# Optimization experiments

Hardware: AMD Instinct MI355X
Metric: run time of the kernel (lower is better)

## Reference

```python
import jax, jax.numpy as jnp
import numpy as np

B, D, H, C = 8192, 384, 256, 6
K_MIN, K_MAX = 4, 16
LN_EPS = 1e-5


def setup_inputs() -> dict:
    key = jax.random.key(0)
    ks = jax.random.split(key, 6)
    s = lambda k, shape: (jax.random.normal(k, shape, jnp.float32) * 0.05)
    return {
        "x": jax.random.normal(ks[0], (B, D), jnp.float32),
        "W_proj": s(ks[1], (D, H)), "b_proj": jnp.zeros((H,), jnp.float32),
        "W_tau": s(ks[2], (D, 1)), "b_tau": jnp.zeros((1,), jnp.float32),
        "W_res": s(ks[3], (H, H)), "b_res": jnp.zeros((H,), jnp.float32),
        "ln_g": jnp.ones((H,), jnp.float32), "ln_b": jnp.zeros((H,), jnp.float32),
        "W_fc": s(ks[4], (H, C)), "b_fc": jnp.zeros((C,), jnp.float32),
    }


def reference(x, W_proj, b_proj, W_tau, b_tau, W_res, b_res, ln_g, ln_b, W_fc, b_fc):
    # adaptive k per sample (torch path casts to int -> non-differentiable)
    tau = jax.nn.sigmoid(x @ W_tau + b_tau)[:, 0]                      # [B]
    k = jax.lax.stop_gradient(
        jnp.clip(jnp.round(K_MAX - (K_MAX - K_MIN) * tau), 1, K_MAX)
    ).astype(jnp.int32)                                                # [B]

    # pairwise squared distances (same nearest-neighbor ordering as cdist)
    sq = jnp.sum(x * x, axis=-1)                                       # [B]
    d2 = sq[:, None] + sq[None, :] - 2.0 * (x @ x.T)                   # [B,B]
    _, idx = jax.lax.top_k(-jax.lax.stop_gradient(d2), K_MAX)          # [B,K_MAX] nearest (incl. self)

    h = jax.nn.relu(x @ W_proj + b_proj)                               # [B,H]

    # ragged top-k mean via fixed K_MAX gather + position mask
    gathered = h[idx]                                                  # [B,K_MAX,H]
    mask = (jnp.arange(K_MAX)[None, :] < k[:, None]).astype(h.dtype)   # [B,K_MAX]
    agg = jnp.einsum('bkh,bk->bh', gathered, mask) / k[:, None].astype(h.dtype)

    r = jax.nn.relu(agg @ W_res + b_res)                               # [B,H]
    z = h + r
    mu = jnp.mean(z, axis=-1, keepdims=True)
    var = jnp.var(z, axis=-1, keepdims=True)
    zn = (z - mu) / jnp.sqrt(var + LN_EPS)
    return (zn * ln_g + ln_b) @ W_fc + b_fc                            # [B,C]
```

## Files before the change

kernel.cpp:

```cpp
#include <hip/hip_runtime.h>
#include <hip/hip_fp16.h>
#include <math.h>

#define NROWS 8192
#define DDIM 384
#define HDIM 256
#define CDIM 6
#define LN_EPS 1e-5f
#define DSTR 138

typedef short bf16x8 __attribute__((ext_vector_type(8)));
typedef float f32x4 __attribute__((ext_vector_type(4)));
typedef unsigned short u16x8 __attribute__((ext_vector_type(8)));
typedef unsigned short u16x4 __attribute__((ext_vector_type(4)));
typedef unsigned short u16x2 __attribute__((ext_vector_type(2)));

__device__ __forceinline__ bool dj_better(float d1, int j1, float d2, int j2) {
    return (d1 < d2) || (d1 == d2 && j1 < j2);
}

__device__ __forceinline__ unsigned int umin_(unsigned int a, unsigned int b) { return a < b ? a : b; }
__device__ __forceinline__ unsigned int umax_(unsigned int a, unsigned int b) { return a > b ? a : b; }

__device__ __forceinline__ unsigned short map16f(float v) {
    union { _Float16 f; unsigned short u; } c;
    c.f = (_Float16)v;
    unsigned short b = c.u;
    return (unsigned short)(b ^ (unsigned short)((((short)b) >> 15) | 0x8000));
}

__device__ __forceinline__ unsigned short rne_bf16(float v) {
    unsigned int u = __float_as_uint(v);
    u += 0x7fffu + ((u >> 16) & 1u);
    return (unsigned short)(u >> 16);
}

__device__ __forceinline__ void ins8(
    unsigned int& s0, unsigned int& s1, unsigned int& s2, unsigned int& s3,
    unsigned int& s4, unsigned int& s5, unsigned int& s6, unsigned int& s7,
    unsigned int& m, unsigned int key)
{
    if (key < m) {
        s0 = (s0 == m) ? key : s0;
        s1 = (s1 == m) ? key : s1;
        s2 = (s2 == m) ? key : s2;
        s3 = (s3 == m) ? key : s3;
        s4 = (s4 == m) ? key : s4;
        s5 = (s5 == m) ? key : s5;
        s6 = (s6 == m) ? key : s6;
        s7 = (s7 == m) ? key : s7;
        m = umax_(umax_(umax_(s0, s1), umax_(s2, s3)),
                  umax_(umax_(s4, s5), umax_(s6, s7)));
    }
}

__device__ __forceinline__ unsigned int max8_(
    unsigned int s0, unsigned int s1, unsigned int s2, unsigned int s3,
    unsigned int s4, unsigned int s5, unsigned int s6, unsigned int s7)
{
    return umax_(umax_(umax_(s0, s1), umax_(s2, s3)),
                 umax_(umax_(s4, s5), umax_(s6, s7)));
}

__global__ void __launch_bounds__(256) prep_kernel(
    const float* __restrict__ x, const float* __restrict__ W_tau,
    const float* __restrict__ b_tau, unsigned short* __restrict__ xb,
    float* __restrict__ sq, int* __restrict__ kk,
    const float* __restrict__ Wp, unsigned short* __restrict__ wpT,
    const float* __restrict__ Wr, unsigned short* __restrict__ wrT)
{
    int tid = threadIdx.x;
    if (blockIdx.x < NROWS / 4) {
        int wave = tid >> 6, lane = tid & 63;
        int row = blockIdx.x * 4 + wave;
        const float* xr = x + (size_t)row * DDIM;
        unsigned short* xbr = xb + (size_t)row * DDIM;
        float s = 0.f, tp = 0.f;
        #pragma unroll
        for (int q = 0; q < 6; ++q) {
            float v = xr[lane + 64 * q];
            xbr[lane + 64 * q] = rne_bf16(v);
            s = fmaf(v, v, s);
            tp = fmaf(v, W_tau[lane + 64 * q], tp);
        }
        #pragma unroll
        for (int off = 32; off > 0; off >>= 1) {
            s += __shfl_xor(s, off);
            tp += __shfl_xor(tp, off);
        }
        if (lane == 0) {
            sq[row] = s;
            float u = tp + b_tau[0];
            float tau = 1.f / (1.f + expf(-u));
            float kf = rintf(16.f - 12.f * tau);
            int k = (int)kf;
            k = min(16, max(1, k));
            kk[row] = k;
        }
    } else {
        int i = (blockIdx.x - NROWS / 4) * 256 + tid;
        if (i < DDIM * HDIM) {
            int k = i / HDIM, n = i % HDIM;
            wpT[(size_t)n * DDIM + k] = rne_bf16(Wp[i]);
        } else {
            int j = i - DDIM * HDIM;
            if (j < HDIM * HDIM) {
                int k = j / HDIM, n = j % HDIM;
                wrT[(size_t)n * HDIM + k] = rne_bf16(Wr[j]);
            }
        }
    }
}

__global__ void __launch_bounds__(256) mfma_gemm_bias_relu_kernel(
    const unsigned short* __restrict__ A, const unsigned short* __restrict__ WT,
    const float* __restrict__ bias, float* __restrict__ out,
    unsigned short* __restrict__ hb, int K)
{
    __shared__ unsigned short Abuf[128 * 32];
    __shared__ unsigned short Bbuf[128 * 32];

    const int tid = threadIdx.x;
    const int wave = tid >> 6;
    const int rowbase = blockIdx.x * 128;
    const int nbase = blockIdx.y * 128;
    const int lane = tid & 63;
    const int wr = (wave >> 1) * 64;
    const int wc = (wave & 1) * 64;
    const int m16 = lane & 15;
    const int kq = lane >> 4;

    const int er0 = tid >> 2;
    const int er1 = 64 + (tid >> 2);
    const int eko = tid & 3;

    f32x4 acc[4][4];
    #pragma unroll
    for (int a = 0; a < 4; ++a)
        #pragma unroll
        for (int b = 0; b < 4; ++b)
            acc[a][b] = (f32x4){0.f, 0.f, 0.f, 0.f};

    for (int kb = 0; kb < K / 32; ++kb) {
        const int k0 = kb * 32;
        __syncthreads();
        __builtin_amdgcn_global_load_lds(
            (const __attribute__((address_space(1))) void*)(A + (size_t)(rowbase + er0) * K + k0 + eko * 8),
            (__attribute__((address_space(3))) void*)((char*)Abuf + (wave * 64) * 16), 16, 0, 0);
        __builtin_amdgcn_global_load_lds(
            (const __attribute__((address_space(1))) void*)(A + (size_t)(rowbase + er1) * K + k0 + eko * 8),
            (__attribute__((address_space(3))) void*)((char*)Abuf + (256 + wave * 64) * 16), 16, 0, 0);
        __builtin_amdgcn_global_load_lds(
            (const __attribute__((address_space(1))) void*)(WT + (size_t)(nbase + er0) * K + k0 + eko * 8),
            (__attribute__((address_space(3))) void*)((char*)Bbuf + (wave * 64) * 16), 16, 0, 0);
        __builtin_amdgcn_global_load_lds(
            (const __attribute__((address_space(1))) void*)(WT + (size_t)(nbase + er1) * K + k0 + eko * 8),
            (__attribute__((address_space(3))) void*)((char*)Bbuf + (256 + wave * 64) * 16), 16, 0, 0);
        __syncthreads();

        bf16x8 af[4], bfr[4];
        #pragma unroll
        for (int s = 0; s < 4; ++s) {
            af[s]  = *(const bf16x8*)&Abuf[(wr + s * 16 + m16) * 32 + kq * 8];
            bfr[s] = *(const bf16x8*)&Bbuf[(wc + s * 16 + m16) * 32 + kq * 8];
        }
        #pragma unroll
        for (int si = 0; si < 4; ++si)
            #pragma unroll
            for (int sj = 0; sj < 4; ++sj)
                acc[si][sj] = __builtin_amdgcn_mfma_f32_16x16x32_bf16(
                    af[si], bfr[sj], acc[si][sj], 0, 0, 0);
    }

    #pragma unroll
    for (int sj = 0; sj < 4; ++sj) {
        int c = nbase + wc + sj * 16 + m16;
        float bc = bias[c];
        #pragma unroll
        for (int si = 0; si < 4; ++si) {
            int r = rowbase + wr + si * 16 + kq * 4;
            #pragma unroll
            for (int v = 0; v < 4; ++v) {
                float val = fmaxf(acc[si][sj][v] + bc, 0.f);
                out[(size_t)(r + v) * HDIM + c] = val;
                if (hb) hb[(size_t)(r + v) * HDIM + c] = rne_bf16(val);
            }
        }
    }
}

__global__ void __launch_bounds__(256) dist_topk_kernel(
    const unsigned short* __restrict__ xb, const float* __restrict__ sq,
    unsigned int* __restrict__ keys)
{
    __shared__ unsigned short Abuf[128 * 32];
    __shared__ unsigned short Bbuf[128 * 32];
    __shared__ __align__(16) unsigned short Dt[128 * DSTR];

    int t = blockIdx.x;
    int bi = (int)((sqrtf(8.f * (float)t + 1.f) - 1.f) * 0.5f);
    while ((bi + 1) * (bi + 2) / 2 <= t) ++bi;
    while (bi * (bi + 1) / 2 > t) --bi;
    int bj = t - bi * (bi + 1) / 2;

    const int tid = threadIdx.x;
    const int wave = tid >> 6;
    const int lane = tid & 63;
    const int rowbase = bi * 128;
    const int colbase = bj * 128;
    const int wr = (wave >> 1) * 64;
    const int wc = (wave & 1) * 64;
    const int m16 = lane & 15;
    const int kq = lane >> 4;

    const int er0 = tid >> 2;
    const int er1 = 64 + (tid >> 2);
    const int eko = tid & 3;

    f32x4 acc[4][4];
    #pragma unroll
    for (int a = 0; a < 4; ++a)
        #pragma unroll
        for (int b = 0; b < 4; ++b)
            acc[a][b] = (f32x4){0.f, 0.f, 0.f, 0.f};

    for (int kb = 0; kb < DDIM / 32; ++kb) {
        const int k0 = kb * 32;
        __syncthreads();
        __builtin_amdgcn_global_load_lds(
            (const __attribute__((address_space(1))) void*)(xb + (size_t)(rowbase + er0) * DDIM + k0 + eko * 8),
            (__attribute__((address_space(3))) void*)((char*)Abuf + (wave * 64) * 16), 16, 0, 0);
        __builtin_amdgcn_global_load_lds(
            (const __attribute__((address_space(1))) void*)(xb + (size_t)(rowbase + er1) * DDIM + k0 + eko * 8),
            (__attribute__((address_space(3))) void*)((char*)Abuf + (256 + wave * 64) * 16), 16, 0, 0);
        __builtin_amdgcn_global_load_lds(
            (const __attribute__((address_space(1))) void*)(xb + (size_t)(colbase + er0) * DDIM + k0 + eko * 8),
            (__attribute__((address_space(3))) void*)((char*)Bbuf + (wave * 64) * 16), 16, 0, 0);
        __builtin_amdgcn_global_load_lds(
            (const __attribute__((address_space(1))) void*)(xb + (size_t)(colbase + er1) * DDIM + k0 + eko * 8),
            (__attribute__((address_space(3))) void*)((char*)Bbuf + (256 + wave * 64) * 16), 16, 0, 0);
        __syncthreads();

        bf16x8 af[4], bfr[4];
        #pragma unroll
        for (int s = 0; s < 4; ++s) {
            af[s]  = *(const bf16x8*)&Abuf[(wr + s * 16 + m16) * 32 + kq * 8];
            bfr[s] = *(const bf16x8*)&Bbuf[(wc + s * 16 + m16) * 32 + kq * 8];
        }
        #pragma unroll
        for (int si = 0; si < 4; ++si)
            #pragma unroll
            for (int sj = 0; sj < 4; ++sj)
                acc[si][sj] = __builtin_amdgcn_mfma_f32_16x16x32_bf16(
                    af[si], bfr[sj], acc[si][sj], 0, 0, 0);
    }

    const int sr = tid >> 1;
    const int seg = tid & 1;

    {
        float sqc[4];
        #pragma unroll
        for (int sj = 0; sj < 4; ++sj) sqc[sj] = sq[colbase + wc + sj * 16 + m16];
        #pragma unroll
        for (int si = 0; si < 4; ++si)
            #pragma unroll
            for (int sj = 0; sj < 4; ++sj) {
                int r = wr + si * 16 + kq * 4;
                int c = wc + sj * 16 + m16;
                #pragma unroll
                for (int v = 0; v < 4; ++v)
                    Dt[(r + v) * DSTR + c] = map16f(sqc[sj] - 2.0f * acc[si][sj][v]);
            }
        __syncthreads();

        const unsigned short* rowp = &Dt[sr * DSTR + seg * 64];
        const int cb0 = colbase + seg * 64;
        u16x8 c0 = *(const u16x8*)rowp;
        unsigned int s0 = ((unsigned int)c0[0] << 13) | (unsigned int)(cb0 + 0);
        unsigned int s1 = ((unsigned int)c0[1] << 13) | (unsigned int)(cb0 + 1);
        unsigned int s2 = ((unsigned int)c0[2] << 13) | (unsigned int)(cb0 + 2);
        unsigned int s3 = ((unsigned int)c0[3] << 13) | (unsigned int)(cb0 + 3);
        unsigned int s4 = ((unsigned int)c0[4] << 13) | (unsigned int)(cb0 + 4);
        unsigned int s5 = ((unsigned int)c0[5] << 13) | (unsigned int)(cb0 + 5);
        unsigned int s6 = ((unsigned int)c0[6] << 13) | (unsigned int)(cb0 + 6);
        unsigned int s7 = ((unsigned int)c0[7] << 13) | (unsigned int)(cb0 + 7);
        unsigned int m = max8_(s0, s1, s2, s3, s4, s5, s6, s7);
        #pragma unroll
        for (int i = 1; i < 8; ++i) {
            u16x8 ch = *(const u16x8*)(rowp + i * 8);
            u16x4 g4 = __builtin_elementwise_min(
                __builtin_shufflevector(ch, ch, 0, 1, 2, 3),
                __builtin_shufflevector(ch, ch, 4, 5, 6, 7));
            u16x2 g2 = __builtin_elementwise_min(
                __builtin_shufflevector(g4, g4, 0, 1),
                __builtin_shufflevector(g4, g4, 2, 3));
            unsigned int gmin = umin_((unsigned int)g2[0], (unsigned int)g2[1]);
            if ((gmin << 13) < m) {
                int cb = cb0 + i * 8;
                #pragma unroll
                for (int e = 0; e < 8; ++e)
                    ins8(s0, s1, s2, s3, s4, s5, s6, s7, m,
                         ((unsigned int)ch[e] << 13) | (unsigned int)(cb + e));
            }
        }
        size_t kb = (size_t)(rowbase + sr) * 1024 + (size_t)bj * 16 + seg * 8;
        uint4 o0; o0.x = s0; o0.y = s1; o0.z = s2; o0.w = s3;
        uint4 o1; o1.x = s4; o1.y = s5; o1.z = s6; o1.w = s7;
        *(uint4*)&keys[kb] = o0;
        *(uint4*)&keys[kb + 4] = o1;
    }

    if (bi != bj) {
        __syncthreads();
        #pragma unroll
        for (int si = 0; si < 4; ++si) {
            float4 sqr4 = *(const float4*)&sq[rowbase + wr + si * 16 + kq * 4];
            float srw[4] = {sqr4.x, sqr4.y, sqr4.z, sqr4.w};
            #pragma unroll
            for (int sj = 0; sj < 4; ++sj) {
                int r = wr + si * 16 + kq * 4;
                int c = wc + sj * 16 + m16;
                unsigned short h4[4];
                #pragma unroll
                for (int v = 0; v < 4; ++v)
                    h4[v] = map16f(srw[v] - 2.0f * acc[si][sj][v]);
                *(unsigned long long*)&Dt[c * DSTR + r] = *(unsigned long long*)h4;
            }
        }
        __syncthreads();

        const unsigned short* rowp = &Dt[sr * DSTR + seg * 64];
        const int cb0 = rowbase + seg * 64;
        u16x8 c0 = *(const u16x8*)rowp;
        unsigned int s0 = ((unsigned int)c0[0] << 13) | (unsigned int)(cb0 + 0);
        unsigned int s1 = ((unsigned int)c0[1] << 13) | (unsigned int)(cb0 + 1);
        unsigned int s2 = ((unsigned int)c0[2] << 13) | (unsigned int)(cb0 + 2);
        unsigned int s3 = ((unsigned int)c0[3] << 13) | (unsigned int)(cb0 + 3);
        unsigned int s4 = ((unsigned int)c0[4] << 13) | (unsigned int)(cb0 + 4);
        unsigned int s5 = ((unsigned int)c0[5] << 13) | (unsigned int)(cb0 + 5);
        unsigned int s6 = ((unsigned int)c0[6] << 13) | (unsigned int)(cb0 + 6);
        unsigned int s7 = ((unsigned int)c0[7] << 13) | (unsigned int)(cb0 + 7);
        unsigned int m = max8_(s0, s1, s2, s3, s4, s5, s6, s7);
        #pragma unroll
        for (int i = 1; i < 8; ++i) {
            u16x8 ch = *(const u16x8*)(rowp + i * 8);
            u16x4 g4 = __builtin_elementwise_min(
                __builtin_shufflevector(ch, ch, 0, 1, 2, 3),
                __builtin_shufflevector(ch, ch, 4, 5, 6, 7));
            u16x2 g2 = __builtin_elementwise_min(
                __builtin_shufflevector(g4, g4, 0, 1),
                __builtin_shufflevector(g4, g4, 2, 3));
            unsigned int gmin = umin_((unsigned int)g2[0], (unsigned int)g2[1]);
            if ((gmin << 13) < m) {
                int cb = cb0 + i * 8;
                #pragma unroll
                for (int e = 0; e < 8; ++e)
                    ins8(s0, s1, s2, s3, s4, s5, s6, s7, m,
                         ((unsigned int)ch[e] << 13) | (unsigned int)(cb + e));
            }
        }
        size_t kb = (size_t)(colbase + sr) * 1024 + (size_t)bi * 16 + seg * 8;
        uint4 o0; o0.x = s0; o0.y = s1; o0.z = s2; o0.w = s3;
        uint4 o1; o1.x = s4; o1.y = s5; o1.z = s6; o1.w = s7;
        *(uint4*)&keys[kb] = o0;
        *(uint4*)&keys[kb + 4] = o1;
    }
}

__global__ void __launch_bounds__(256) topk_rescore_agg_kernel(
    const unsigned int* __restrict__ keys, const float* __restrict__ x,
    const float* __restrict__ sq, const int* __restrict__ kk,
    const unsigned short* __restrict__ hb, unsigned short* __restrict__ aggb)
{
    const int w = threadIdx.x >> 6;
    const int row = blockIdx.x * 4 + w;
    const int lane = threadIdx.x & 63;
    __shared__ int sidx[4][16];

    const uint4* kp = (const uint4*)(keys + (size_t)row * 1024 + lane * 16);
    uint4 v0 = kp[0], v1 = kp[1];
    unsigned int s0 = v0.x, s1 = v0.y, s2 = v0.z, s3 = v0.w;
    unsigned int s4 = v1.x, s5 = v1.y, s6 = v1.z, s7 = v1.w;
    unsigned int m = max8_(s0, s1, s2, s3, s4, s5, s6, s7);
    #pragma unroll
    for (int q = 2; q < 4; ++q) {
        uint4 v = kp[q];
        unsigned int gmin = umin_(umin_(v.x, v.y), umin_(v.z, v.w));
        if (gmin < m) {
            ins8(s0, s1, s2, s3, s4, s5, s6, s7, m, v.x);
            ins8(s0, s1, s2, s3, s4, s5, s6, s7, m, v.y);
            ins8(s0, s1, s2, s3, s4, s5, s6, s7, m, v.z);
            ins8(s0, s1, s2, s3, s4, s5, s6, s7, m, v.w);
        }
    }
    unsigned int lmin = umin_(umin_(umin_(s0, s1), umin_(s2, s3)),
                              umin_(umin_(s4, s5), umin_(s6, s7)));
    unsigned int myout = 0;
    for (int t = 0; t < 32; ++t) {
        unsigned int wv = lmin;
        #pragma unroll
        for (int off = 32; off > 0; off >>= 1)
            wv = umin_(wv, (unsigned int)__shfl_xor((int)wv, off));
        if (lane == t) myout = wv;
        if (lmin == wv) {
            s0 = (s0 == wv) ? 0xFFFFFFFFu : s0;
            s1 = (s1 == wv) ? 0xFFFFFFFFu : s1;
            s2 = (s2 == wv) ? 0xFFFFFFFFu : s2;
            s3 = (s3 == wv) ? 0xFFFFFFFFu : s3;
            s4 = (s4 == wv) ? 0xFFFFFFFFu : s4;
            s5 = (s5 == wv) ? 0xFFFFFFFFu : s5;
            s6 = (s6 == wv) ? 0xFFFFFFFFu : s6;
            s7 = (s7 == wv) ? 0xFFFFFFFFu : s7;
            lmin = umin_(umin_(umin_(s0, s1), umin_(s2, s3)),
                         umin_(umin_(s4, s5), umin_(s6, s7)));
        }
    }
    int myj = __shfl((int)(myout & 8191u), lane & 31);

    const int l32 = lane & 31;
    const int half = lane >> 5;
    float xr[12];
    #pragma unroll
    for (int q = 0; q < 12; ++q) xr[q] = x[(size_t)row * DDIM + l32 + 32 * q];
    float sqrow = sq[row];
    float myd = 0.f;
    for (int i = 0; i < 16; ++i) {
        int c0 = 2 * i + half;
        int j = __shfl(myj, c0);
        const float* xc = x + (size_t)j * DDIM;
        float p = 0.f;
        #pragma unroll
        for (int q = 0; q < 12; ++q) p = fmaf(xr[q], xc[l32 + 32 * q], p);
        #pragma unroll
        for (int off = 16; off > 0; off >>= 1) p += __shfl_xor(p, off);
        float d = sqrow + sq[j] - 2.f * p;
        float d_even = __shfl(d, 0);
        float d_odd  = __shfl(d, 32);
        if (lane == 2 * i)     myd = d_even;
        if (lane == 2 * i + 1) myd = d_odd;
    }
    int rank = 0;
    for (int t = 0; t < 32; ++t) {
        float dt = __shfl(myd, t); int jt = __shfl(myj, t);
        if (dj_better(dt, jt, myd, myj)) ++rank;
    }
    if (lane < 32 && rank < 16) sidx[w][rank] = myj;
    __syncthreads();

    int k = kk[row];
    float a0 = 0.f, a1 = 0.f, a2 = 0.f, a3 = 0.f;
    for (int t = 0; t < k; ++t) {
        uint2 v = *(const uint2*)(hb + (size_t)sidx[w][t] * HDIM + lane * 4);
        a0 += __uint_as_float(v.x << 16);
        a1 += __uint_as_float(v.x & 0xFFFF0000u);
        a2 += __uint_as_float(v.y << 16);
        a3 += __uint_as_float(v.y & 0xFFFF0000u);
    }
    float inv = 1.f / (float)k;
    unsigned int b0 = rne_bf16(a0 * inv);
    unsigned int b1 = rne_bf16(a1 * inv);
    unsigned int b2 = rne_bf16(a2 * inv);
    unsigned int b3 = rne_bf16(a3 * inv);
    uint2 o; o.x = b0 | (b1 << 16); o.y = b2 | (b3 << 16);
    *(uint2*)(aggb + (size_t)row * HDIM + lane * 4) = o;
}

__global__ void __launch_bounds__(256) ln_fc_kernel(
    const float* __restrict__ h, const float* __restrict__ r,
    const float* __restrict__ g, const float* __restrict__ bb,
    const float* __restrict__ W_fc, const float* __restrict__ b_fc,
    float* __restrict__ out)
{
    const int row = blockIdx.x * 4 + (threadIdx.x >> 6);
    const int lane = threadIdx.x & 63;
    const float* hp = h + (size_t)row * HDIM;
    const float* rp = r + (size_t)row * HDIM;

    float z[4];
    #pragma unroll
    for (int q = 0; q < 4; ++q)
        z[q] = hp[lane + 64 * q] + rp[lane + 64 * q];

    float s = z[0] + z[1] + z[2] + z[3];
    float s2 = z[0]*z[0] + z[1]*z[1] + z[2]*z[2] + z[3]*z[3];
    #pragma unroll
    for (int off = 32; off > 0; off >>= 1) {
        s += __shfl_xor(s, off);
        s2 += __shfl_xor(s2, off);
    }
    float mu = s / 256.f;
    float rstd = rsqrtf(s2 / 256.f - mu * mu + LN_EPS);

    float p[6] = {0.f, 0.f, 0.f, 0.f, 0.f, 0.f};
    #pragma unroll
    for (int q = 0; q < 4; ++q) {
        int i = lane + 64 * q;
        float val = (z[q] - mu) * rstd * g[i] + bb[i];
        #pragma unroll
        for (int c = 0; c < 6; ++c)
            p[c] = fmaf(val, W_fc[i * 6 + c], p[c]);
    }
    #pragma unroll
    for (int c = 0; c < 6; ++c)
        #pragma unroll
        for (int off = 32; off > 0; off >>= 1) p[c] += __shfl_xor(p[c], off);

    if (lane < 6) {
        float o = p[0];
        o = (lane == 1) ? p[1] : o;
        o = (lane == 2) ? p[2] : o;
        o = (lane == 3) ? p[3] : o;
        o = (lane == 4) ? p[4] : o;
        o = (lane == 5) ? p[5] : o;
        out[(size_t)row * CDIM + lane] = o + b_fc[lane];
    }
}

extern "C" void kernel_launch(void* const* d_in, const int* in_sizes, int n_in,
                              void* d_out, int out_size, void* d_ws, size_t ws_size,
                              hipStream_t stream) {
    const float* x      = (const float*)d_in[0];
    const float* W_proj = (const float*)d_in[1];
    const float* b_proj = (const float*)d_in[2];
    const float* W_tau  = (const float*)d_in[3];
    const float* b_tau  = (const float*)d_in[4];
    const float* W_res  = (const float*)d_in[5];
    const float* b_res  = (const float*)d_in[6];
    const float* ln_g   = (const float*)d_in[7];
    const float* ln_b   = (const float*)d_in[8];
    const float* W_fc   = (const float*)d_in[9];
    const float* b_fc   = (const float*)d_in[10];
    float* out = (float*)d_out;

    char* ws = (char*)d_ws;
    float* sq   = (float*)ws;                        ws += (size_t)NROWS * 4;
    int*   kk   = (int*)ws;                          ws += (size_t)NROWS * 4;
    float* h    = (float*)ws;                        ws += (size_t)NROWS * HDIM * 4;
    float* r    = (float*)ws;                        ws += (size_t)NROWS * HDIM * 4;
    unsigned short* xb   = (unsigned short*)ws;      ws += (size_t)NROWS * DDIM * 2;
    unsigned short* hbuf = (unsigned short*)ws;      ws += (size_t)NROWS * HDIM * 2;
    unsigned short* aggb = (unsigned short*)ws;      ws += (size_t)NROWS * HDIM * 2;
    unsigned short* wpT  = (unsigned short*)ws;      ws += (size_t)DDIM * HDIM * 2;
    unsigned short* wrT  = (unsigned short*)ws;      ws += (size_t)HDIM * HDIM * 2;
    ws = (char*)(((size_t)ws + 255) & ~(size_t)255);
    unsigned int* keys = (unsigned int*)ws;          ws += (size_t)NROWS * 1024 * 4;

    const int prepW = (DDIM * HDIM + HDIM * HDIM + 255) / 256;
    prep_kernel<<<NROWS / 4 + prepW, 256, 0, stream>>>(
        x, W_tau, b_tau, xb, sq, kk, W_proj, wpT, W_res, wrT);
    mfma_gemm_bias_relu_kernel<<<dim3(NROWS / 128, HDIM / 128), 256, 0, stream>>>(
        xb, wpT, b_proj, h, hbuf, DDIM);
    dist_topk_kernel<<<(NROWS/128) * (NROWS/128 + 1) / 2, 256, 0, stream>>>(xb, sq, keys);
    topk_rescore_agg_kernel<<<NROWS / 4, 256, 0, stream>>>(keys, x, sq, kk, hbuf, aggb);
    mfma_gemm_bias_relu_kernel<<<dim3(NROWS / 128, HDIM / 128), 256, 0, stream>>>(
        aggb, wrT, b_res, r, (unsigned short*)nullptr, HDIM);
    ln_fc_kernel<<<NROWS / 4, 256, 0, stream>>>(h, r, ln_g, ln_b, W_fc, b_fc, out);
}
```

Baseline: 239.1 us.

## Refine only ambiguous kNN candidates near the k-th boundary using fp16 scores

Instead of recomputing exact fp32 distances for all 32 approximate candidates and fully ranking them, the kernel decodes the fp16-mapped screening distances, accepts candidates clearly inside the k-th boundary by a margin, and recomputes exact distances only for candidates within the ambiguity band. Exact ranking is applied only among these ambiguous candidates to fill the remaining slots. This aims to cut the per-row gather and dot-product work of the refinement stage. It risks wrong neighbor sets if the fixed margin is too small for the fp16/bf16 screening error.

```diff
diff --git a/kernel.cpp b/kernel.cpp
--- a/kernel.cpp
+++ b/kernel.cpp
@@ -27,6 +27,13 @@
     c.f = (_Float16)v;
     unsigned short b = c.u;
     return (unsigned short)(b ^ (unsigned short)((((short)b) >> 15) | 0x8000));
+}
+
+__device__ __forceinline__ float unmap16(unsigned int m16b) {
+    unsigned short fb = (m16b & 0x8000u) ? (unsigned short)(m16b ^ 0x8000u)
+                                         : (unsigned short)(~m16b);
+    union { unsigned short u; _Float16 f; } cv; cv.u = fb;
+    return (float)cv.f;
 }
 
 __device__ __forceinline__ unsigned short rne_bf16(float v) {
@@ -416,39 +423,61 @@
                          umin_(umin_(s4, s5), umin_(s6, s7)));
         }
     }
-    int myj = __shfl((int)(myout & 8191u), lane & 31);
-
-    const int l32 = lane & 31;
-    const int half = lane >> 5;
-    float xr[12];
-    #pragma unroll
-    for (int q = 0; q < 12; ++q) xr[q] = x[(size_t)row * DDIM + l32 + 32 * q];
-    float sqrow = sq[row];
-    float myd = 0.f;
-    for (int i = 0; i < 16; ++i) {
-        int c0 = 2 * i + half;
-        int j = __shfl(myj, c0);
-        const float* xc = x + (size_t)j * DDIM;
-        float p = 0.f;
-        #pragma unroll
-        for (int q = 0; q < 12; ++q) p = fmaf(xr[q], xc[l32 + 32 * q], p);
-        #pragma unroll
-        for (int off = 16; off > 0; off >>= 1) p += __shfl_xor(p, off);
-        float d = sqrow + sq[j] - 2.f * p;
-        float d_even = __shfl(d, 0);
-        float d_odd  = __shfl(d, 32);
-        if (lane == 2 * i)     myd = d_even;
-        if (lane == 2 * i + 1) myd = d_odd;
-    }
-    int rank = 0;
-    for (int t = 0; t < 32; ++t) {
-        float dt = __shfl(myd, t); int jt = __shfl(myj, t);
-        if (dj_better(dt, jt, myd, myj)) ++rank;
-    }
-    if (lane < 32 && rank < 16) sidx[w][rank] = myj;
+    int myj = (int)(myout & 8191u);
+    float dscr = (lane < 32) ? unmap16(myout >> 13) : INFINITY;
+
+    const float EPS2 = 2.5f;
+    const int k = kk[row];
+    float d_k   = __shfl(dscr, k);
+    float d_km1 = __shfl(dscr, k - 1);
+    bool cin = false, amb = false;
+    if (lane < 32) {
+        if (lane < k) { cin = (dscr + EPS2 <= d_k); amb = !cin; }
+        else          { amb = (dscr < d_km1 + EPS2); }
+    }
+    unsigned long long cinmask = __ballot(cin);
+    unsigned long long ambmask = __ballot(amb);
+    int n_in = __popcll(cinmask);
+    int msel = k - n_in;
+
+    float d_ex = 0.f;
+    if (msel > 0) {
+        float xr[6];
+        #pragma unroll
+        for (int q = 0; q < 6; ++q) xr[q] = x[(size_t)row * DDIM + lane + 64 * q];
+        float sqrow = sq[row];
+        unsigned long long mm = ambmask;
+        while (mm) {
+            int c = (int)(__ffsll(mm) - 1);
+            mm &= mm - 1;
+            int j = __shfl(myj, c);
+            const float* xc = x + (size_t)j * DDIM;
+            float p = 0.f;
+            #pragma unroll
+            for (int q = 0; q < 6; ++q) p = fmaf(xr[q], xc[lane + 64 * q], p);
+            #pragma unroll
+            for (int off = 32; off > 0; off >>= 1) p += __shfl_xor(p, off);
+            float d = sqrow + sq[j] - 2.f * p;
+            if (lane == c) d_ex = d;
+        }
+        int selrank = 0;
+        unsigned long long mm2 = ambmask;
+        while (mm2) {
+            int u = (int)(__ffsll(mm2) - 1);
+            mm2 &= mm2 - 1;
+            float du = __shfl(d_ex, u);
+            int ju = __shfl(myj, u);
+            if (u != lane && dj_better(du, ju, d_ex, myj)) ++selrank;
+        }
+        if (amb && selrank < msel)
+            sidx[w][n_in + selrank] = myj;
+    }
+    if (cin) {
+        int pos = __popcll(cinmask & ((1ull << lane) - 1ull));
+        sidx[w][pos] = myj;
+    }
     __syncthreads();
 
-    int k = kk[row];
     float a0 = 0.f, a1 = 0.f, a2 = 0.f, a3 = 0.f;
     for (int t = 0; t < k; ++t) {
         uint2 v = *(const uint2*)(hb + (size_t)sidx[w][t] * HDIM + lane * 4);
```

Result: faster. 229.2 us (-4.1%).
